# Performance work log

Measured on AMD Instinct MI355X. Metric: run time of the kernel, lower is better.

The kernel has to match this reference:

```python
import jax, jax.numpy as jnp
import numpy as np

COST_PROB = 1.0
COST_HEAT = 1.0


def _cost_blocks(prob, label, heat, gt):
    """Diagonal blocks of the matcher cost: C[b] = cost_heat*L1cdist(heat[b], gt[b]) + cost_prob*(1 - prob[b][:, label[b]]).
    Only these blocks are consumed by the per-batch linear_sum_assignment in the original module.
    Returns [bs, nq, ngt]."""
    bs, nq, _ = prob.shape
    ngt = gt.shape[1]
    # L1 cdist per batch: [bs, nq, ngt]
    cost_h = jnp.abs(heat[:, :, None, :] - gt[:, None, :, :]).sum(-1)
    idx = jnp.broadcast_to(label[:, None, :], (bs, nq, ngt))
    cls_prob = jnp.take_along_axis(prob, idx, axis=2)  # prob[b, q, label[b, g]]
    cost_p = 1.0 - cls_prob
    return COST_HEAT * cost_h + COST_PROB * cost_p


def _lsap(cost):
    """Exact rectangular LSAP (Jonker-Volgenant shortest augmenting path, same algorithm as
    scipy.optimize.linear_sum_assignment). cost is [n, m] with n <= m (here n=ngt, m=nq).
    Returns (row_ind, col_ind) matching scipy's output on the transposed [m, n] matrix:
    row_ind = matched query indices (sorted ascending), col_ind = corresponding gt indices."""
    n, m = cost.shape
    INF = jnp.array(jnp.inf, cost.dtype)

    def solve_row(cur_row, carry):
        u, v, col4row, row4col = carry

        # --- Dijkstra search for shortest augmenting path from cur_row ---
        def dij_cond(st):
            return st[6] < 0

        def dij_body(st):
            i, minVal, SR, SC, shortest, path, sink = st
            SR = SR.at[i].set(True)
            lowest = minVal + cost[i] - u[i] - v  # reduced costs along row i, shape [m]
            upd = (~SC) & (lowest < shortest)
            shortest = jnp.where(upd, lowest, shortest)
            path = jnp.where(upd, i, path)
            masked = jnp.where(SC, INF, shortest)
            j = jnp.argmin(masked).astype(jnp.int32)
            minVal = masked[j]
            SC = SC.at[j].set(True)
            r = row4col[j]
            sink = jnp.where(r < 0, j, jnp.int32(-1))
            i = jnp.where(r < 0, i, r)
            return (i, minVal, SR, SC, shortest, path, sink)

        init = (jnp.int32(cur_row), jnp.array(0.0, cost.dtype),
                jnp.zeros((n,), bool), jnp.zeros((m,), bool),
                jnp.full((m,), INF), jnp.zeros((m,), jnp.int32), jnp.int32(-1))
        _, minVal, SR, SC, shortest, path, sink = jax.lax.while_loop(dij_cond, dij_body, init)

        # --- dual updates ---
        rows = jnp.arange(n)
        u = u.at[cur_row].add(minVal)
        u = u + jnp.where(SR & (rows != cur_row), minVal - shortest[col4row], jnp.array(0.0, cost.dtype))
        v = v - jnp.where(SC, minVal - shortest, jnp.array(0.0, cost.dtype))

        # --- augment along the alternating path back from sink ---
        def aug_cond(st):
            return ~st[3]

        def aug_body(st):
            j, c4r, r4c, _ = st
            i = path[j]
            r4c = r4c.at[j].set(i)
            prev = c4r[i]
            c4r = c4r.at[i].set(j)
            return (prev, c4r, r4c, i == jnp.int32(cur_row))

        _, col4row, row4col, _ = jax.lax.while_loop(
            aug_cond, aug_body, (sink, col4row, row4col, jnp.array(False)))
        return (u, v, col4row, row4col)

    carry0 = (jnp.zeros((n,), cost.dtype), jnp.zeros((m,), cost.dtype),
              jnp.full((n,), -1, jnp.int32), jnp.full((m,), -1, jnp.int32))
    _, _, col4row, _ = jax.lax.fori_loop(0, n, solve_row, carry0)
    order = jnp.argsort(col4row)          # gt indices ordered by matched query index
    return col4row[order], order.astype(jnp.int32)


def setup_inputs() -> dict:
    key = jax.random.key(0)
    k1, k2, k3, k4 = jax.random.split(key, 4)
    bs, nq, ngt, D, ncls = 16, 64, 32, 4096, 33
    prob = jax.random.uniform(k1, (bs, nq, ncls), jnp.float32)
    label = jax.random.randint(k2, (bs, ngt), 0, ncls, jnp.int32)
    heat = jax.random.uniform(k3, (bs, nq, D), jnp.float32)
    gt = jax.random.uniform(k4, (bs, ngt, D), jnp.float32)
    return {"prob": prob, "label": label, "heat": heat, "gt": gt}


def reference(prob, label, heat, gt):
    C = _cost_blocks(prob, label, heat, gt)           # [bs, nq, ngt]
    rows, cols = jax.vmap(_lsap)(jnp.swapaxes(C, 1, 2))  # solve on [ngt, nq] per sample
    return rows, cols                                  # each [bs, ngt]: (query idx sorted, gt idx)
```

## Files before the change

kernel.cpp:

```cpp
#include <hip/hip_runtime.h>
#include <hip/hip_bf16.h>

#define BS   16
#define NQ   64
#define NGT  32
#define DIM  4096
#define NCLS 33

#define QT      8
#define NCHUNK  8
#define CHUNK   (DIM / NCHUNK)

__global__ __launch_bounds__(256) void cost_kernel(
    const float* __restrict__ heat, const float* __restrict__ gt,
    float* __restrict__ Cp)
{
    __shared__ float hrow[QT][CHUNK];
    const int bid  = blockIdx.x;
    const int b    = bid & 15;
    const int rest = bid >> 4;
    const int qt   = rest & (NQ / QT - 1);
    const int c    = rest >> 3;
    const int q0   = qt * QT;

    const float* hbase = heat + ((size_t)(b * NQ + q0)) * DIM + c * CHUNK;
    for (int i = threadIdx.x; i < QT * CHUNK / 4; i += 256) {
        int r = i >> 7;
        int k = i & 127;
        ((float4*)hrow[r])[k] = ((const float4*)(hbase + (size_t)r * DIM))[k];
    }
    __syncthreads();

    const int wave = threadIdx.x >> 6;
    const int lane = threadIdx.x & 63;
    const int g0 = wave * 8;
    const float* gbase = gt + ((size_t)(b * NGT + g0)) * DIM + c * CHUNK;

    float acc[8][QT];
    #pragma unroll
    for (int g = 0; g < 8; ++g)
        #pragma unroll
        for (int q = 0; q < QT; ++q) acc[g][q] = 0.f;

    for (int i = lane; i < CHUNK / 4; i += 64) {
        float4 hv[QT];
        #pragma unroll
        for (int q = 0; q < QT; ++q) hv[q] = ((float4*)hrow[q])[i];
        #pragma unroll
        for (int g = 0; g < 8; ++g) {
            float4 gv = ((const float4*)(gbase + (size_t)g * DIM))[i];
            #pragma unroll
            for (int q = 0; q < QT; ++q) {
                acc[g][q] += fabsf(hv[q].x - gv.x) + fabsf(hv[q].y - gv.y) +
                             fabsf(hv[q].z - gv.z) + fabsf(hv[q].w - gv.w);
            }
        }
    }

    float r[64];
    #pragma unroll
    for (int k = 0; k < 64; ++k) r[k] = acc[k >> 3][k & 7];
    #pragma unroll
    for (int n = 64, m = 1; n > 1; n >>= 1, m <<= 1) {
        #pragma unroll
        for (int k = 0; k < 32; ++k) {
            if (k < n / 2) {
                float a  = r[2 * k], bb = r[2 * k + 1];
                bool  hi = (lane & m) != 0;
                float keep = hi ? bb : a;
                float send = hi ? a : bb;
                r[k] = keep + __shfl_xor(send, m);
            }
        }
    }
    {
        int gl = lane >> 3, ql = lane & 7;
        Cp[(((size_t)(b * NQ + (q0 + ql))) * NGT + (g0 + gl)) * NCHUNK + c] = r[0];
    }
}

__device__ __forceinline__ float dppmin(float x, const int ctrl) {
    int t;
    switch (ctrl) {
        case 0xB1:  t = __builtin_amdgcn_update_dpp(0, __float_as_int(x), 0xB1,  0xf, 0xf, true); break;
        case 0x4E:  t = __builtin_amdgcn_update_dpp(0, __float_as_int(x), 0x4E,  0xf, 0xf, true); break;
        case 0x141: t = __builtin_amdgcn_update_dpp(0, __float_as_int(x), 0x141, 0xf, 0xf, true); break;
        default:    t = __builtin_amdgcn_update_dpp(0, __float_as_int(x), 0x140, 0xf, 0xf, true); break;
    }
    return fminf(x, __int_as_float(t));
}
__device__ __forceinline__ float rdlane_f(float x, int l) {
    return __int_as_float(__builtin_amdgcn_readlane(__float_as_int(x), l));
}

__global__ __launch_bounds__(256) void lsap_kernel(
    const float* __restrict__ Cp, const float* __restrict__ prob,
    const int* __restrict__ label, int* __restrict__ out)
{
    __shared__ float cost[NGT * NQ];
    const int b = blockIdx.x;
    const int tid = threadIdx.x;

    for (int idx = tid; idx < NQ * NGT; idx += 256) {
        int q = idx & 63;
        int g = idx >> 6;
        const float* p = &Cp[(((size_t)(b * NQ + q)) * NGT + g) * NCHUNK];
        float4 v4a = *(const float4*)p;
        float4 v4b = *(const float4*)(p + 4);
        int lb = label[b * NGT + g];
        float cpr = 1.0f - prob[((size_t)(b * NQ + q)) * NCLS + lb];
        float s = ((v4a.x + v4a.y) + (v4a.z + v4a.w)) +
                  ((v4b.x + v4b.y) + (v4b.z + v4b.w));
        cost[g * 64 + q] = s + cpr;
    }
    __syncthreads();
    if (tid >= 64) return;
    const int lane = tid;

    const float INF = __builtin_inff();
    float v = 0.f;
    float u_reg = 0.f;
    int c4r = -1;
    int r4c = -1;

    for (int cur = 0; cur < NGT; ++cur) {
        unsigned SRmask = 0;
        float shortest = INF;
        int pathv = 0;
        bool SC = false;
        float minVal = 0.f;
        int i = cur;
        int sink = -1;

        while (sink < 0) {
            SRmask |= (1u << i);
            float ci = cost[(i << 6) + lane];
            float ui = rdlane_f(u_reg, i);
            float lowest = minVal + ci - ui - v;
            if (!SC && lowest < shortest) { shortest = lowest; pathv = i; }
            float masked = SC ? INF : shortest;
            float x = masked;
            x = dppmin(x, 0xB1);
            x = dppmin(x, 0x4E);
            x = dppmin(x, 0x141);
            x = dppmin(x, 0x140);
            float mv = rdlane_f(x, 0);
            mv = fminf(mv, rdlane_f(x, 16));
            mv = fminf(mv, rdlane_f(x, 32));
            mv = fminf(mv, rdlane_f(x, 48));
            unsigned long long ball = __ballot(masked == mv);
            int j = __ffsll(ball) - 1;
            minVal = mv;
            if (lane == j) SC = true;
            int rr = __builtin_amdgcn_readlane(r4c, j);
            if (rr < 0) sink = j;
            else        i = rr;
        }

        if (lane == cur) u_reg += minVal;
        {
            float shc = __shfl(shortest, c4r & 63);
            bool rowupd = (lane < NGT) && (lane != cur) && ((SRmask >> lane) & 1u);
            if (rowupd) u_reg += minVal - shc;
        }
        if (SC) v -= minVal - shortest;

        int j = sink;
        while (true) {
            int ii = __builtin_amdgcn_readlane(pathv, j);
            if (lane == j) r4c = ii;
            int prev = __builtin_amdgcn_readlane(c4r, ii);
            if (lane == ii) c4r = j;
            if (ii == cur) break;
            j = prev;
        }
    }

    int cc = c4r;
    int rank = 0;
    for (int t = 0; t < NGT; ++t) {
        int ct = __shfl(c4r, t);
        rank += (ct < cc) ? 1 : 0;
    }
    if (lane < NGT) {
        out[b * NGT + rank] = cc;
        out[BS * NGT + b * NGT + rank] = lane;
    }
}

extern "C" void kernel_launch(void* const* d_in, const int* in_sizes, int n_in,
                              void* d_out, int out_size, void* d_ws, size_t ws_size,
                              hipStream_t stream) {
    const float* prob  = (const float*)d_in[0];
    const int*   label = (const int*)d_in[1];
    const float* heat  = (const float*)d_in[2];
    const float* gt    = (const float*)d_in[3];
    int* out = (int*)d_out;
    float* Cp = (float*)d_ws;

    cost_kernel<<<dim3(BS * (NQ / QT) * NCHUNK), dim3(256), 0, stream>>>(heat, gt, Cp);
    lsap_kernel<<<dim3(BS), dim3(256), 0, stream>>>(Cp, prob, label, out);
}
```

Measured before the change: 41.49 us.

## Warm-start LSAP with greedy row-minimum assignment and faster DPP wave-min

Before the augmenting-path loop, the kernel sets each row's dual to its row minimum and greedily assigns each row to its argmin column when that column is still free. Rows already matched this way skip the Dijkstra search, which cuts the number of serial shortest-path searches. The wave-wide minimum now uses row_bcast DPP steps and a single readlane instead of four readlanes. Because the final assignment is still optimal, output differs only if ties occur, and the remaining searches may run longer.

```diff
diff --git a/kernel.cpp b/kernel.cpp
--- a/kernel.cpp
+++ b/kernel.cpp
@@ -79,18 +79,23 @@
     }
 }
 
-__device__ __forceinline__ float dppmin(float x, const int ctrl) {
-    int t;
-    switch (ctrl) {
-        case 0xB1:  t = __builtin_amdgcn_update_dpp(0, __float_as_int(x), 0xB1,  0xf, 0xf, true); break;
-        case 0x4E:  t = __builtin_amdgcn_update_dpp(0, __float_as_int(x), 0x4E,  0xf, 0xf, true); break;
-        case 0x141: t = __builtin_amdgcn_update_dpp(0, __float_as_int(x), 0x141, 0xf, 0xf, true); break;
-        default:    t = __builtin_amdgcn_update_dpp(0, __float_as_int(x), 0x140, 0xf, 0xf, true); break;
-    }
+template<int CTRL>
+__device__ __forceinline__ float dppmin_t(float x) {
+    int t = __builtin_amdgcn_update_dpp(__float_as_int(x), __float_as_int(x),
+                                        CTRL, 0xf, 0xf, false);
     return fminf(x, __int_as_float(t));
 }
 __device__ __forceinline__ float rdlane_f(float x, int l) {
     return __int_as_float(__builtin_amdgcn_readlane(__float_as_int(x), l));
+}
+__device__ __forceinline__ float wavemin64(float x) {
+    x = dppmin_t<0xB1>(x);
+    x = dppmin_t<0x4E>(x);
+    x = dppmin_t<0x141>(x);
+    x = dppmin_t<0x140>(x);
+    x = dppmin_t<0x142>(x);
+    x = dppmin_t<0x143>(x);
+    return rdlane_f(x, 63);
 }
 
 __global__ __launch_bounds__(256) void lsap_kernel(
@@ -123,7 +128,32 @@
     int c4r = -1;
     int r4c = -1;
 
+    {
+        float xg[NGT]; float mg[NGT]; int jg[NGT];
+        #pragma unroll
+        for (int g = 0; g < NGT; ++g) xg[g] = cost[(g << 6) + lane];
+        #pragma unroll
+        for (int g = 0; g < NGT; ++g) {
+            float m = wavemin64(xg[g]);
+            unsigned long long ball = __ballot(xg[g] == m);
+            jg[g] = __ffsll(ball) - 1;
+            mg[g] = m;
+        }
+        #pragma unroll
+        for (int g = 0; g < NGT; ++g) {
+            int j = jg[g];
+            int rtaken = __builtin_amdgcn_readlane(r4c, j);
+            if (rtaken < 0) {
+                if (lane == j) r4c = g;
+                if (lane == g) c4r = j;
+            }
+            if (lane == g) u_reg = mg[g];
+        }
+    }
+
     for (int cur = 0; cur < NGT; ++cur) {
+        if (__builtin_amdgcn_readlane(c4r, cur) >= 0) continue;
+
         unsigned SRmask = 0;
         float shortest = INF;
         int pathv = 0;
@@ -139,15 +169,7 @@
             float lowest = minVal + ci - ui - v;
             if (!SC && lowest < shortest) { shortest = lowest; pathv = i; }
             float masked = SC ? INF : shortest;
-            float x = masked;
-            x = dppmin(x, 0xB1);
-            x = dppmin(x, 0x4E);
-            x = dppmin(x, 0x141);
-            x = dppmin(x, 0x140);
-            float mv = rdlane_f(x, 0);
-            mv = fminf(mv, rdlane_f(x, 16));
-            mv = fminf(mv, rdlane_f(x, 32));
-            mv = fminf(mv, rdlane_f(x, 48));
+            float mv = wavemin64(masked);
             unsigned long long ball = __ballot(masked == mv);
             int j = __ffsll(ball) - 1;
             minVal = mv;
```

After: 37.48 us. 9.7% less time.
